# Kernel tuning notes

Measured on AMD Instinct MI355X. Metric: run time of the kernel, lower is better.

Reference implementation:

```python
import jax, jax.numpy as jnp
import numpy as np
import math

B, I, H = 8192, 1024, 1024


def setup_inputs() -> dict:
    key = jax.random.key(0)
    ks = jax.random.split(key, 16)
    stdv = 1.0 / math.sqrt(H)
    u = lambda k, shape: jax.random.uniform(k, shape, jnp.float32, -stdv, stdv)
    inp = {
        'xt': jax.random.normal(ks[0], (B, I), jnp.float32),
        'cx': jax.random.normal(ks[1], (B, H), jnp.float32),
        'hx': jax.random.normal(ks[2], (B, H), jnp.float32),
        'w_fg': u(ks[3], (H, I)), 'w_ig': u(ks[4], (H, I)),
        'w_og': u(ks[5], (H, I)), 'w_ci': u(ks[6], (H, I)),
        'r_fg': u(ks[7], (H, H)), 'r_ig': u(ks[8], (H, H)),
        'r_og': u(ks[9], (H, H)), 'r_ci': u(ks[10], (H, H)),
        'b_fg': u(ks[11], (H,)), 'b_ig': u(ks[12], (H,)),
        'b_og': u(ks[13], (H,)), 'b_ci': u(ks[14], (H,)),
    }
    return inp


def reference(xt, cx, hx, w_fg, w_ig, w_og, w_ci, r_fg, r_ig, r_og, r_ci,
              b_fg, b_ig, b_og, b_ci):
    # Fuse the four input matmuls and four recurrent matmuls into two GEMMs.
    W = jnp.concatenate([w_fg, w_ig, w_og, w_ci], axis=0)  # [4H, I]
    R = jnp.concatenate([r_fg, r_ig, r_og, r_ci], axis=0)  # [4H, H]
    b = jnp.concatenate([b_fg, b_ig, b_og, b_ci], axis=0)  # [4H]
    gates = xt @ W.T + hx @ R.T + b                         # [B, 4H]
    f, i, o, g = jnp.split(gates, 4, axis=-1)
    ft = jax.nn.sigmoid(f)
    it = jax.nn.sigmoid(i)
    ot = jax.nn.sigmoid(o)
    ct = ft * cx + it * jnp.tanh(g)
    ht = ot * jnp.tanh(ct)
    return (ht, ct)
```

## Files before the change

### kernel.cpp

```cpp
#include <hip/hip_runtime.h>

#define B_DIM 8192
#define H_DIM 1024
#define K_DIM 2048
#define N_DIM 4096
#define BH (B_DIM * H_DIM)
#define NT 32
#define TSZ (256 * 64)
#define HALFT (128 * 64)

using frag_ab = __attribute__((ext_vector_type(8))) short;
using frag_cd = __attribute__((ext_vector_type(4))) float;

__device__ __forceinline__ unsigned short f2bf(float f) {
  union { float f; unsigned u; } x; x.f = f;
  return (unsigned short)((x.u + 0x7fffu + ((x.u >> 16) & 1u)) >> 16);
}

__global__ __launch_bounds__(256) void convert_A_kernel(
    const float* __restrict__ xt, const float* __restrict__ hx,
    unsigned short* __restrict__ Ab) {
  int tid = blockIdx.x * 256 + threadIdx.x;
  int flat = tid * 4;
  int m = flat >> 11;
  int k = flat & 2047;
  const float* src = (k < 1024) ? (xt + m * 1024 + k)
                                : (hx + m * 1024 + (k - 1024));
  float4 v = *reinterpret_cast<const float4*>(src);
  ushort4 o;
  o.x = f2bf(v.x); o.y = f2bf(v.y); o.z = f2bf(v.z); o.w = f2bf(v.w);
  *reinterpret_cast<ushort4*>(Ab + flat) = o;
}

__global__ __launch_bounds__(256) void convert_B_kernel(
    const float* __restrict__ w0, const float* __restrict__ w1,
    const float* __restrict__ w2, const float* __restrict__ w3,
    const float* __restrict__ r0, const float* __restrict__ r1,
    const float* __restrict__ r2, const float* __restrict__ r3,
    unsigned short* __restrict__ Bb) {
  int tid = blockIdx.x * 256 + threadIdx.x;
  int flat = tid * 4;
  int n = flat >> 11;
  int k = flat & 2047;
  int tile = n >> 8, c = n & 255;
  int gate = (c >> 4) & 3;
  int h = tile * 64 + ((c >> 6) << 4) + (c & 15);
  const float* wb = (gate == 0) ? w0 : (gate == 1) ? w1 : (gate == 2) ? w2 : w3;
  const float* rb = (gate == 0) ? r0 : (gate == 1) ? r1 : (gate == 2) ? r2 : r3;
  const float* src = (k < 1024) ? (wb + h * 1024 + k)
                                : (rb + h * 1024 + (k - 1024));
  float4 v = *reinterpret_cast<const float4*>(src);
  ushort4 o;
  o.x = f2bf(v.x); o.y = f2bf(v.y); o.z = f2bf(v.z); o.w = f2bf(v.w);
  *reinterpret_cast<ushort4*>(Bb + flat) = o;
}

__device__ __forceinline__ void gload_lds16(const void* g, void* l) {
  __builtin_amdgcn_global_load_lds(
      (const __attribute__((address_space(1))) unsigned int*)g,
      (__attribute__((address_space(3))) unsigned int*)l, 16, 0, 0);
}

__device__ __forceinline__ frag_ab ldsr(const unsigned short* buf, int byteoff) {
  return *reinterpret_cast<const frag_ab*>(
      reinterpret_cast<const char*>(buf) + byteoff);
}

__device__ __forceinline__ float fast_sigmoid(float x) {
  return 1.f / (1.f + __expf(-x));
}
__device__ __forceinline__ float fast_tanh(float x) {
  return 1.f - 2.f / (__expf(2.f * x) + 1.f);
}

#define CBAR asm volatile("" ::: "memory")
#define SBAR do { CBAR; __builtin_amdgcn_s_barrier(); CBAR; } while (0)
#define SCHED0 __builtin_amdgcn_sched_barrier(0)

#define TILE_BODY(Ac, Bc, Anx, Bnx, tt, S1, S2, S3, S4, VM2, VM0)             \
  {                                                                            \
       \
    _Pragma("unroll") for (int m = 0; m < 4; ++m)                              \
        Af0[m] = ldsr(Ac, (arow + m * 16) * 128 + c0);                         \
    _Pragma("unroll") for (int n = 0; n < 4; ++n)                              \
        Bf0[n] = ldsr(Bc, (brow + n * 16) * 128 + c0);                         \
    if (S1) stage(Bg + 128 * K_DIM + (size_t)((tt) + 1) * 64, (Bnx) + HALFT);  \
    __builtin_amdgcn_s_setprio(1);                                             \
    _Pragma("unroll") for (int m = 0; m < 4; ++m)                              \
        _Pragma("unroll") for (int n = 0; n < 4; ++n)                          \
            acc[m][n] = __builtin_amdgcn_mfma_f32_16x16x32_bf16(               \
                Af0[m], Bf0[n], acc[m][n], 0, 0, 0);                           \
    __builtin_amdgcn_s_setprio(0);                                             \
    SCHED0;                                                                    \
    SBAR;                                                                      \
       \
    _Pragma("unroll") for (int m = 0; m < 4; ++m)                              \
        Af1[m] = ldsr(Ac, (arow + m * 16) * 128 + c1);                         \
    _Pragma("unroll") for (int n = 0; n < 4; ++n)                              \
        Bf1[n] = ldsr(Bc, (brow + n * 16) * 128 + c1);                         \
    if (S2) stage(Ag + (size_t)((tt) + 1) * 64, (Anx));                        \
    __builtin_amdgcn_s_setprio(1);                                             \
    _Pragma("unroll") for (int m = 0; m < 4; ++m)                              \
        _Pragma("unroll") for (int n = 0; n < 4; ++n)                          \
            acc[m][n] = __builtin_amdgcn_mfma_f32_16x16x32_bf16(               \
                Af1[m], Bf1[n], acc[m][n], 0, 0, 0);                           \
    __builtin_amdgcn_s_setprio(0);                                             \
    SCHED0;                                                                    \
    SBAR;                                                                      \
          \
    _Pragma("unroll") for (int m = 0; m < 4; ++m)                              \
        Af0[m] = ldsr(Ac, (arow + 64 + m * 16) * 128 + c0);                    \
    if (S3) stage(Ag + (size_t)((tt) + 1) * 64 + 128 * K_DIM, (Anx) + HALFT);  \
    __builtin_amdgcn_s_setprio(1);                                             \
    _Pragma("unroll") for (int m = 0; m < 4; ++m)                              \
        _Pragma("unroll") for (int n = 0; n < 4; ++n)                          \
            acc[4 + m][n] = __builtin_amdgcn_mfma_f32_16x16x32_bf16(           \
                Af0[m], Bf0[n], acc[4 + m][n], 0, 0, 0);                       \
    __builtin_amdgcn_s_setprio(0);                                             \
    SCHED0;                                                                    \
    SBAR;                                                                      \
     \
    _Pragma("unroll") for (int m = 0; m < 4; ++m)                              \
        Af1[m] = ldsr(Ac, (arow + 64 + m * 16) * 128 + c1);                    \
    if (S4) stage(Bg + (size_t)((tt) + 2) * 64, (Bc));                         \
    __builtin_amdgcn_s_setprio(1);                                             \
    _Pragma("unroll") for (int m = 0; m < 4; ++m)                              \
        _Pragma("unroll") for (int n = 0; n < 4; ++n)                          \
            acc[4 + m][n] = __builtin_amdgcn_mfma_f32_16x16x32_bf16(           \
                Af1[m], Bf1[n], acc[4 + m][n], 0, 0, 0);                       \
    __builtin_amdgcn_s_setprio(0);                                             \
    if (VM2) asm volatile("s_waitcnt vmcnt(2)" ::: "memory");                  \
    if (VM0) asm volatile("s_waitcnt vmcnt(0)" ::: "memory");                  \
    SCHED0;                                                                    \
    SBAR;                                                                      \
  }

__global__ __launch_bounds__(512, 2) void lstm_gemm_kernel(
    const unsigned short* __restrict__ Ab,
    const unsigned short* __restrict__ Bb,
    const float* __restrict__ cx,
    const float* __restrict__ b_f, const float* __restrict__ b_i,
    const float* __restrict__ b_o, const float* __restrict__ b_g,
    float* __restrict__ out) {
  extern __shared__ unsigned short smem[];
  unsigned short* const As0 = smem;
  unsigned short* const As1 = smem + TSZ;
  unsigned short* const Bs0 = smem + 2 * TSZ;
  unsigned short* const Bs1 = smem + 3 * TSZ;

  const int bid = blockIdx.x;
  const int swz = (bid & 7) * 64 + (bid >> 3);
  const int bm = swz >> 4;
  const int bn = swz & 15;

  const int tid = threadIdx.x;
  const int lane = tid & 63;
  const int wid = tid >> 6;
  const int wr = wid >> 2, wc = wid & 3;
  const int ln = lane & 15, kh = lane >> 4;

  const unsigned short* Ag = Ab + (size_t)(bm * 256) * K_DIM;
  const unsigned short* Bg = Bb + (size_t)(bn * 256) * K_DIM;

  const size_t gs0 = (size_t)(wid * 16 + (lane >> 3)) * K_DIM +
                     (((lane & 7) ^ (lane >> 3)) << 3);
  const size_t gs1 = gs0 + (size_t)8 * K_DIM;
  const int ld0 = wid * 2048 + lane * 16;
  const int ld1 = ld0 + 1024;
  auto stage = [&](const unsigned short* g, unsigned short* l) {
    gload_lds16(g + gs0, reinterpret_cast<char*>(l) + ld0);
    gload_lds16(g + gs1, reinterpret_cast<char*>(l) + ld1);
  };

  const int inv = (ln & 7) << 4;
  const int c0 = (kh * 16) ^ inv;
  const int c1 = (64 + kh * 16) ^ inv;
  const int arow = wr * 128 + ln;
  const int brow = wc * 64 + ln;

  frag_cd acc[8][4] = {};
  frag_ab Af0[4], Af1[4], Bf0[4], Bf1[4];

  stage(Ag, As0);
  stage(Ag + 128 * K_DIM, As0 + HALFT);
  stage(Bg, Bs0);
  stage(Bg + 128 * K_DIM, Bs0 + HALFT);
  stage(Bg + 64, Bs1);
  asm volatile("s_waitcnt vmcnt(2)" ::: "memory");
  SBAR;

  for (int u = 0; u < 15; ++u) {
    const int e = 2 * u;
    TILE_BODY(As0, Bs0, As1, Bs1, e, 1, 1, 1, 1, 1, 0);
    TILE_BODY(As1, Bs1, As0, Bs0, e + 1, 1, 1, 1, 1, 1, 0);
  }
  TILE_BODY(As0, Bs0, As1, Bs1, 30, 1, 1, 1, 0, 0, 1);
  TILE_BODY(As1, Bs1, As0, Bs0, 31, 0, 0, 0, 0, 0, 0);

  const int hcol = bn * 64 + wc * 16 + ln;
  const float bfv = b_f[hcol], biv = b_i[hcol], bov = b_o[hcol], bgv = b_g[hcol];
  const int row_base = bm * 256 + wr * 128 + kh * 4;
#pragma unroll
  for (int mi = 0; mi < 8; ++mi) {
#pragma unroll
    for (int j = 0; j < 4; ++j) {
      const int row = row_base + mi * 16 + j;
      float fp = acc[mi][0][j] + bfv;
      float ip = acc[mi][1][j] + biv;
      float op = acc[mi][2][j] + bov;
      float gp = acc[mi][3][j] + bgv;
      float ft = fast_sigmoid(fp);
      float it = fast_sigmoid(ip);
      float ot = fast_sigmoid(op);
      float gt = fast_tanh(gp);
      float cold = cx[(size_t)row * H_DIM + hcol];
      float ct = ft * cold + it * gt;
      float ht = ot * fast_tanh(ct);
      out[(size_t)row * H_DIM + hcol] = ht;
      out[BH + (size_t)row * H_DIM + hcol] = ct;
    }
  }
}

extern "C" void kernel_launch(void* const* d_in, const int* in_sizes, int n_in,
                              void* d_out, int out_size, void* d_ws, size_t ws_size,
                              hipStream_t stream) {
  const float* xt   = (const float*)d_in[0];
  const float* cxp  = (const float*)d_in[1];
  const float* hx   = (const float*)d_in[2];
  const float* w_fg = (const float*)d_in[3];
  const float* w_ig = (const float*)d_in[4];
  const float* w_og = (const float*)d_in[5];
  const float* w_ci = (const float*)d_in[6];
  const float* r_fg = (const float*)d_in[7];
  const float* r_ig = (const float*)d_in[8];
  const float* r_og = (const float*)d_in[9];
  const float* r_ci = (const float*)d_in[10];
  const float* b_fg = (const float*)d_in[11];
  const float* b_ig = (const float*)d_in[12];
  const float* b_og = (const float*)d_in[13];
  const float* b_ci = (const float*)d_in[14];

  unsigned short* Abf = (unsigned short*)d_ws;
  unsigned short* Bbf = Abf + (size_t)B_DIM * K_DIM;
  float* out = (float*)d_out;

  convert_A_kernel<<<dim3(B_DIM * K_DIM / 4 / 256), dim3(256), 0, stream>>>(
      xt, hx, Abf);
  convert_B_kernel<<<dim3(N_DIM * K_DIM / 4 / 256), dim3(256), 0, stream>>>(
      w_fg, w_ig, w_og, w_ci, r_fg, r_ig, r_og, r_ci, Bbf);
  lstm_gemm_kernel<<<dim3((B_DIM / 256) * (N_DIM / 256)), dim3(512),
                     131072, stream>>>(
      Abf, Bbf, cxp, b_fg, b_ig, b_og, b_ci, out);
}
```

Before: 157.5 us.

## Load A fragments directly from global in MFMA-ready layout, stage only B in LDS

The A-conversion kernel now writes bf16 activations in a fragment-tiled layout, so each wave loads its MFMA A operands straight from global memory into registers. Only B goes through LDS, which halves shared memory (64KB instead of 128KB) and cuts per-tile barriers from four to one. The cost is that A is read from global by each of the four column waves with no LDS sharing, relying on L2/L1 hits. The global-load latency also lands directly in the MFMA loop, with the vmcnt waits tuned to match.

```diff
diff --git a/kernel.cpp b/kernel.cpp
--- a/kernel.cpp
+++ b/kernel.cpp
@@ -6,11 +6,12 @@
 #define N_DIM 4096
 #define BH (B_DIM * H_DIM)
 #define NT 32
-#define TSZ (256 * 64)
-#define HALFT (128 * 64)
+#define BTSZ (256 * 64)
+#define HALFB (128 * 64)
 
 using frag_ab = __attribute__((ext_vector_type(8))) short;
 using frag_cd = __attribute__((ext_vector_type(4))) float;
+using short8 = __attribute__((ext_vector_type(8))) short;
 
 __device__ __forceinline__ unsigned short f2bf(float f) {
   union { float f; unsigned u; } x; x.f = f;
@@ -19,17 +20,21 @@
 
 __global__ __launch_bounds__(256) void convert_A_kernel(
     const float* __restrict__ xt, const float* __restrict__ hx,
-    unsigned short* __restrict__ Ab) {
-  int tid = blockIdx.x * 256 + threadIdx.x;
-  int flat = tid * 4;
-  int m = flat >> 11;
-  int k = flat & 2047;
-  const float* src = (k < 1024) ? (xt + m * 1024 + k)
-                                : (hx + m * 1024 + (k - 1024));
-  float4 v = *reinterpret_cast<const float4*>(src);
-  ushort4 o;
-  o.x = f2bf(v.x); o.y = f2bf(v.y); o.z = f2bf(v.z); o.w = f2bf(v.w);
-  *reinterpret_cast<ushort4*>(Ab + flat) = o;
+    unsigned short* __restrict__ At) {
+  int g = blockIdx.x * 256 + threadIdx.x;
+  int mt = g >> 12;
+  int kt = (g >> 6) & 63;
+  int l = g & 63;
+  int row = mt * 16 + (l & 15);
+  int col = kt * 32 + (l >> 4) * 8;
+  const float* src = (col < 1024) ? (xt + (size_t)row * 1024 + col)
+                                  : (hx + (size_t)row * 1024 + (col - 1024));
+  float4 v0 = *reinterpret_cast<const float4*>(src);
+  float4 v1 = *reinterpret_cast<const float4*>(src + 4);
+  short8 o;
+  o[0] = f2bf(v0.x); o[1] = f2bf(v0.y); o[2] = f2bf(v0.z); o[3] = f2bf(v0.w);
+  o[4] = f2bf(v1.x); o[5] = f2bf(v1.y); o[6] = f2bf(v1.z); o[7] = f2bf(v1.w);
+  *reinterpret_cast<short8*>(At + (size_t)g * 8) = o;
 }
 
 __global__ __launch_bounds__(256) void convert_B_kernel(
@@ -77,76 +82,73 @@
 #define SBAR do { CBAR; __builtin_amdgcn_s_barrier(); CBAR; } while (0)
 #define SCHED0 __builtin_amdgcn_sched_barrier(0)
 
-#define TILE_BODY(Ac, Bc, Anx, Bnx, tt, S1, S2, S3, S4, VM2, VM0)             \
+#define TILE_BODY(Bc, Bn, tt, S, P, VMQ)                                       \
   {                                                                            \
-       \
-    _Pragma("unroll") for (int m = 0; m < 4; ++m)                              \
-        Af0[m] = ldsr(Ac, (arow + m * 16) * 128 + c0);                         \
-    _Pragma("unroll") for (int n = 0; n < 4; ++n)                              \
-        Bf0[n] = ldsr(Bc, (brow + n * 16) * 128 + c0);                         \
-    if (S1) stage(Bg + 128 * K_DIM + (size_t)((tt) + 1) * 64, (Bnx) + HALFT);  \
+    if (S) {                                                                   \
+      stage(Bg + (size_t)((tt) + 1) * 64, (Bn));                               \
+      stage(Bg + (size_t)((tt) + 1) * 64 + 128 * K_DIM, (Bn) + HALFB);         \
+    }                                                                          \
+    SCHED0;                        \
+    _Pragma("unroll") for (int n = 0; n < 4; ++n) {                            \
+      Bf[n][0] = ldsr(Bc, (brow + n * 16) * 128 + c0);                         \
+      Bf[n][1] = ldsr(Bc, (brow + n * 16) * 128 + c1);                         \
+    }                                                                          \
+                 \
+    _Pragma("unroll") for (int m = 0; m < 4; ++m)                              \
+        Af1[m] = *reinterpret_cast<const frag_ab*>(                            \
+            awave + (size_t)m * 32768 + (2 * (tt) + 1) * 512);                 \
     __builtin_amdgcn_s_setprio(1);                                             \
     _Pragma("unroll") for (int m = 0; m < 4; ++m)                              \
         _Pragma("unroll") for (int n = 0; n < 4; ++n)                          \
             acc[m][n] = __builtin_amdgcn_mfma_f32_16x16x32_bf16(               \
-                Af0[m], Bf0[n], acc[m][n], 0, 0, 0);                           \
-    __builtin_amdgcn_s_setprio(0);                                             \
-    SCHED0;                                                                    \
-    SBAR;                                                                      \
-       \
-    _Pragma("unroll") for (int m = 0; m < 4; ++m)                              \
-        Af1[m] = ldsr(Ac, (arow + m * 16) * 128 + c1);                         \
-    _Pragma("unroll") for (int n = 0; n < 4; ++n)                              \
-        Bf1[n] = ldsr(Bc, (brow + n * 16) * 128 + c1);                         \
-    if (S2) stage(Ag + (size_t)((tt) + 1) * 64, (Anx));                        \
+                Af0[m], Bf[n][0], acc[m][n], 0, 0, 0);                         \
+    __builtin_amdgcn_s_setprio(0);                                             \
+                                 \
+    _Pragma("unroll") for (int m = 0; m < 4; ++m)                              \
+        Af0[m] = *reinterpret_cast<const frag_ab*>(                            \
+            awave + (size_t)(4 + m) * 32768 + (2 * (tt)) * 512);               \
     __builtin_amdgcn_s_setprio(1);                                             \
     _Pragma("unroll") for (int m = 0; m < 4; ++m)                              \
         _Pragma("unroll") for (int n = 0; n < 4; ++n)                          \
             acc[m][n] = __builtin_amdgcn_mfma_f32_16x16x32_bf16(               \
-                Af1[m], Bf1[n], acc[m][n], 0, 0, 0);                           \
-    __builtin_amdgcn_s_setprio(0);                                             \
-    SCHED0;                                                                    \
-    SBAR;                                                                      \
-          \
-    _Pragma("unroll") for (int m = 0; m < 4; ++m)                              \
-        Af0[m] = ldsr(Ac, (arow + 64 + m * 16) * 128 + c0);                    \
-    if (S3) stage(Ag + (size_t)((tt) + 1) * 64 + 128 * K_DIM, (Anx) + HALFT);  \
+                Af1[m], Bf[n][1], acc[m][n], 0, 0, 0);                         \
+    __builtin_amdgcn_s_setprio(0);                                             \
+                                 \
+    _Pragma("unroll") for (int m = 0; m < 4; ++m)                              \
+        Af1[m] = *reinterpret_cast<const frag_ab*>(                            \
+            awave + (size_t)(4 + m) * 32768 + (2 * (tt) + 1) * 512);           \
     __builtin_amdgcn_s_setprio(1);                                             \
     _Pragma("unroll") for (int m = 0; m < 4; ++m)                              \
         _Pragma("unroll") for (int n = 0; n < 4; ++n)                          \
             acc[4 + m][n] = __builtin_amdgcn_mfma_f32_16x16x32_bf16(           \
-                Af0[m], Bf0[n], acc[4 + m][n], 0, 0, 0);                       \
-    __builtin_amdgcn_s_setprio(0);                                             \
-    SCHED0;                                                                    \
-    SBAR;                                                                      \
-     \
-    _Pragma("unroll") for (int m = 0; m < 4; ++m)                              \
-        Af1[m] = ldsr(Ac, (arow + 64 + m * 16) * 128 + c1);                    \
-    if (S4) stage(Bg + (size_t)((tt) + 2) * 64, (Bc));                         \
+                Af0[m], Bf[n][0], acc[4 + m][n], 0, 0, 0);                     \
+    __builtin_amdgcn_s_setprio(0);                                             \
+                     \
+    if (P) _Pragma("unroll") for (int m = 0; m < 4; ++m)                       \
+        Af0[m] = *reinterpret_cast<const frag_ab*>(                            \
+            awave + (size_t)m * 32768 + (2 * (tt) + 2) * 512);                 \
     __builtin_amdgcn_s_setprio(1);                                             \
     _Pragma("unroll") for (int m = 0; m < 4; ++m)                              \
         _Pragma("unroll") for (int n = 0; n < 4; ++n)                          \
             acc[4 + m][n] = __builtin_amdgcn_mfma_f32_16x16x32_bf16(           \
-                Af1[m], Bf1[n], acc[4 + m][n], 0, 0, 0);                       \
-    __builtin_amdgcn_s_setprio(0);                                             \
-    if (VM2) asm volatile("s_waitcnt vmcnt(2)" ::: "memory");                  \
-    if (VM0) asm volatile("s_waitcnt vmcnt(0)" ::: "memory");                  \
-    SCHED0;                                                                    \
-    SBAR;                                                                      \
+                Af1[m], Bf[n][1], acc[4 + m][n], 0, 0, 0);                     \
+    __builtin_amdgcn_s_setprio(0);                                             \
+    if (VMQ) {                                                                 \
+      asm volatile("s_waitcnt vmcnt(16)" ::: "memory");    \
+      SBAR;                                                                    \
+    }                                                                          \
   }
 
 __global__ __launch_bounds__(512, 2) void lstm_gemm_kernel(
-    const unsigned short* __restrict__ Ab,
+    const unsigned short* __restrict__ At,
     const unsigned short* __restrict__ Bb,
     const float* __restrict__ cx,
     const float* __restrict__ b_f, const float* __restrict__ b_i,
     const float* __restrict__ b_o, const float* __restrict__ b_g,
     float* __restrict__ out) {
   extern __shared__ unsigned short smem[];
-  unsigned short* const As0 = smem;
-  unsigned short* const As1 = smem + TSZ;
-  unsigned short* const Bs0 = smem + 2 * TSZ;
-  unsigned short* const Bs1 = smem + 3 * TSZ;
+  unsigned short* const Bs0 = smem;
+  unsigned short* const Bs1 = smem + BTSZ;
 
   const int bid = blockIdx.x;
   const int swz = (bid & 7) * 64 + (bid >> 3);
@@ -159,7 +161,8 @@
   const int wr = wid >> 2, wc = wid & 3;
   const int ln = lane & 15, kh = lane >> 4;
 
-  const unsigned short* Ag = Ab + (size_t)(bm * 256) * K_DIM;
+  const unsigned short* awave =
+      At + ((size_t)(bm * 16 + wr * 8) * 64) * 512 + lane * 8;
   const unsigned short* Bg = Bb + (size_t)(bn * 256) * K_DIM;
 
   const size_t gs0 = (size_t)(wid * 16 + (lane >> 3)) * K_DIM +
@@ -175,27 +178,26 @@
   const int inv = (ln & 7) << 4;
   const int c0 = (kh * 16) ^ inv;
   const int c1 = (64 + kh * 16) ^ inv;
-  const int arow = wr * 128 + ln;
   const int brow = wc * 64 + ln;
 
   frag_cd acc[8][4] = {};
-  frag_ab Af0[4], Af1[4], Bf0[4], Bf1[4];
-
-  stage(Ag, As0);
-  stage(Ag + 128 * K_DIM, As0 + HALFT);
+  frag_ab Af0[4], Af1[4], Bf[4][2];
+
   stage(Bg, Bs0);
-  stage(Bg + 128 * K_DIM, Bs0 + HALFT);
-  stage(Bg + 64, Bs1);
-  asm volatile("s_waitcnt vmcnt(2)" ::: "memory");
+  stage(Bg + 128 * K_DIM, Bs0 + HALFB);
+#pragma unroll
+  for (int m = 0; m < 4; ++m)
+    Af0[m] = *reinterpret_cast<const frag_ab*>(awave + (size_t)m * 32768);
+  asm volatile("s_waitcnt vmcnt(4)" ::: "memory");
   SBAR;
 
   for (int u = 0; u < 15; ++u) {
     const int e = 2 * u;
-    TILE_BODY(As0, Bs0, As1, Bs1, e, 1, 1, 1, 1, 1, 0);
-    TILE_BODY(As1, Bs1, As0, Bs0, e + 1, 1, 1, 1, 1, 1, 0);
+    TILE_BODY(Bs0, Bs1, e, 1, 1, 1);
+    TILE_BODY(Bs1, Bs0, e + 1, 1, 1, 1);
   }
-  TILE_BODY(As0, Bs0, As1, Bs1, 30, 1, 1, 1, 0, 0, 1);
-  TILE_BODY(As1, Bs1, As0, Bs0, 31, 0, 0, 0, 0, 0, 0);
+  TILE_BODY(Bs0, Bs1, 30, 1, 1, 1);
+  TILE_BODY(Bs1, Bs0, 31, 0, 0, 0);
 
   const int hcol = bn * 64 + wc * 16 + ln;
   const float bfv = b_f[hcol], biv = b_i[hcol], bov = b_o[hcol], bgv = b_g[hcol];
@@ -241,15 +243,15 @@
   const float* b_og = (const float*)d_in[13];
   const float* b_ci = (const float*)d_in[14];
 
-  unsigned short* Abf = (unsigned short*)d_ws;
-  unsigned short* Bbf = Abf + (size_t)B_DIM * K_DIM;
+  unsigned short* Atf = (unsigned short*)d_ws;
+  unsigned short* Bbf = Atf + (size_t)B_DIM * K_DIM;
   float* out = (float*)d_out;
 
-  convert_A_kernel<<<dim3(B_DIM * K_DIM / 4 / 256), dim3(256), 0, stream>>>(
-      xt, hx, Abf);
+  convert_A_kernel<<<dim3(B_DIM * K_DIM / 8 / 256), dim3(256), 0, stream>>>(
+      xt, hx, Atf);
   convert_B_kernel<<<dim3(N_DIM * K_DIM / 4 / 256), dim3(256), 0, stream>>>(
       w_fg, w_ig, w_og, w_ci, r_fg, r_ig, r_og, r_ci, Bbf);
   lstm_gemm_kernel<<<dim3((B_DIM / 256) * (N_DIM / 256)), dim3(512),
-                     131072, stream>>>(
-      Abf, Bbf, cxp, b_fg, b_ig, b_og, b_ci, out);
-}
+                     65536, stream>>>(
+      Atf, Bbf, cxp, b_fg, b_ig, b_og, b_ci, out);
+}
```

Result: slower. 171.1 us (+8.7%).

## Move barriers before MFMA phases and use toggled LDS read pointers

Applied to the files above, without the earlier changes.

Each barrier in the tile body now sits right after the LDS fragment reads and the global-to-LDS stage issue, before the MFMA block, rather than after it. The sched_barrier fences are removed, so the compiler is free to interleave instructions. LDS read addresses become precomputed pointers flipped between double buffers with an XOR of 0x8000, and global source pointers advance incrementally. The aim is to cut address arithmetic and let barrier waits overlap with MFMA issue, at the risk of changing the ordering that protected buffers being overwritten while still in use.

```diff
diff --git a/kernel.cpp b/kernel.cpp
--- a/kernel.cpp
+++ b/kernel.cpp
@@ -61,11 +61,6 @@
       (__attribute__((address_space(3))) unsigned int*)l, 16, 0, 0);
 }
 
-__device__ __forceinline__ frag_ab ldsr(const unsigned short* buf, int byteoff) {
-  return *reinterpret_cast<const frag_ab*>(
-      reinterpret_cast<const char*>(buf) + byteoff);
-}
-
 __device__ __forceinline__ float fast_sigmoid(float x) {
   return 1.f / (1.f + __expf(-x));
 }
@@ -75,54 +70,52 @@
 
 #define CBAR asm volatile("" ::: "memory")
 #define SBAR do { CBAR; __builtin_amdgcn_s_barrier(); CBAR; } while (0)
-#define SCHED0 __builtin_amdgcn_sched_barrier(0)
-
-#define TILE_BODY(Ac, Bc, Anx, Bnx, tt, S1, S2, S3, S4, VM2, VM0)             \
+#define TOGG(p) (p) = (const char*)((size_t)(p) ^ 0x8000)
+
+#define TILE_BODY(Anx, Bnx, Bcur, S1, S2, S3, S4, VM2, VM0)                    \
   {                                                                            \
-       \
-    _Pragma("unroll") for (int m = 0; m < 4; ++m)                              \
-        Af0[m] = ldsr(Ac, (arow + m * 16) * 128 + c0);                         \
+                 \
+    _Pragma("unroll") for (int m = 0; m < 4; ++m)                              \
+        Af0[m] = *reinterpret_cast<const frag_ab*>(rdA0 + m * 2048);           \
     _Pragma("unroll") for (int n = 0; n < 4; ++n)                              \
-        Bf0[n] = ldsr(Bc, (brow + n * 16) * 128 + c0);                         \
-    if (S1) stage(Bg + 128 * K_DIM + (size_t)((tt) + 1) * 64, (Bnx) + HALFT);  \
+        Bf0[n] = *reinterpret_cast<const frag_ab*>(rdB0 + n * 2048);           \
+    if (S1) { stage(gB1, (Bnx) + HALFT); gB1 += 64; }                          \
+    SBAR;                                                                      \
     __builtin_amdgcn_s_setprio(1);                                             \
     _Pragma("unroll") for (int m = 0; m < 4; ++m)                              \
         _Pragma("unroll") for (int n = 0; n < 4; ++n)                          \
             acc[m][n] = __builtin_amdgcn_mfma_f32_16x16x32_bf16(               \
                 Af0[m], Bf0[n], acc[m][n], 0, 0, 0);                           \
     __builtin_amdgcn_s_setprio(0);                                             \
-    SCHED0;                                                                    \
-    SBAR;                                                                      \
-       \
-    _Pragma("unroll") for (int m = 0; m < 4; ++m)                              \
-        Af1[m] = ldsr(Ac, (arow + m * 16) * 128 + c1);                         \
+                                  \
+    _Pragma("unroll") for (int m = 0; m < 4; ++m)                              \
+        Af1[m] = *reinterpret_cast<const frag_ab*>(rdA1 + m * 2048);           \
     _Pragma("unroll") for (int n = 0; n < 4; ++n)                              \
-        Bf1[n] = ldsr(Bc, (brow + n * 16) * 128 + c1);                         \
-    if (S2) stage(Ag + (size_t)((tt) + 1) * 64, (Anx));                        \
+        Bf1[n] = *reinterpret_cast<const frag_ab*>(rdB1 + n * 2048);           \
+    if (S2) { stage(gA0, (Anx)); gA0 += 64; }                                  \
+    SBAR;                                                                      \
     __builtin_amdgcn_s_setprio(1);                                             \
     _Pragma("unroll") for (int m = 0; m < 4; ++m)                              \
         _Pragma("unroll") for (int n = 0; n < 4; ++n)                          \
             acc[m][n] = __builtin_amdgcn_mfma_f32_16x16x32_bf16(               \
                 Af1[m], Bf1[n], acc[m][n], 0, 0, 0);                           \
     __builtin_amdgcn_s_setprio(0);                                             \
-    SCHED0;                                                                    \
-    SBAR;                                                                      \
-          \
-    _Pragma("unroll") for (int m = 0; m < 4; ++m)                              \
-        Af0[m] = ldsr(Ac, (arow + 64 + m * 16) * 128 + c0);                    \
-    if (S3) stage(Ag + (size_t)((tt) + 1) * 64 + 128 * K_DIM, (Anx) + HALFT);  \
+                \
+    _Pragma("unroll") for (int m = 0; m < 4; ++m)                              \
+        Af0[m] = *reinterpret_cast<const frag_ab*>(rdA0 + 8192 + m * 2048);    \
+    if (S3) { stage(gA1, (Anx) + HALFT); gA1 += 64; }                          \
+    SBAR;                                                                      \
     __builtin_amdgcn_s_setprio(1);                                             \
     _Pragma("unroll") for (int m = 0; m < 4; ++m)                              \
         _Pragma("unroll") for (int n = 0; n < 4; ++n)                          \
             acc[4 + m][n] = __builtin_amdgcn_mfma_f32_16x16x32_bf16(           \
                 Af0[m], Bf0[n], acc[4 + m][n], 0, 0, 0);                       \
     __builtin_amdgcn_s_setprio(0);                                             \
-    SCHED0;                                                                    \
-    SBAR;                                                                      \
-     \
-    _Pragma("unroll") for (int m = 0; m < 4; ++m)                              \
-        Af1[m] = ldsr(Ac, (arow + 64 + m * 16) * 128 + c1);                    \
-    if (S4) stage(Bg + (size_t)((tt) + 2) * 64, (Bc));                         \
+        \
+    _Pragma("unroll") for (int m = 0; m < 4; ++m)                              \
+        Af1[m] = *reinterpret_cast<const frag_ab*>(rdA1 + 8192 + m * 2048);    \
+    if (S4) { stage(gB0, (Bcur)); gB0 += 64; }                                 \
+    SBAR;                                                                      \
     __builtin_amdgcn_s_setprio(1);                                             \
     _Pragma("unroll") for (int m = 0; m < 4; ++m)                              \
         _Pragma("unroll") for (int n = 0; n < 4; ++n)                          \
@@ -131,8 +124,7 @@
     __builtin_amdgcn_s_setprio(0);                                             \
     if (VM2) asm volatile("s_waitcnt vmcnt(2)" ::: "memory");                  \
     if (VM0) asm volatile("s_waitcnt vmcnt(0)" ::: "memory");                  \
-    SCHED0;                                                                    \
-    SBAR;                                                                      \
+    TOGG(rdA0); TOGG(rdA1); TOGG(rdB0); TOGG(rdB1);                            \
   }
 
 __global__ __launch_bounds__(512, 2) void lstm_gemm_kernel(
@@ -178,6 +170,16 @@
   const int arow = wr * 128 + ln;
   const int brow = wc * 64 + ln;
 
+  const char* rdA0 = reinterpret_cast<const char*>(As0) + arow * 128 + c0;
+  const char* rdA1 = reinterpret_cast<const char*>(As0) + arow * 128 + c1;
+  const char* rdB0 = reinterpret_cast<const char*>(Bs0) + brow * 128 + c0;
+  const char* rdB1 = reinterpret_cast<const char*>(Bs0) + brow * 128 + c1;
+
+  const unsigned short* gA0 = Ag + 64;
+  const unsigned short* gA1 = Ag + 64 + 128 * K_DIM;
+  const unsigned short* gB1 = Bg + 64 + 128 * K_DIM;
+  const unsigned short* gB0 = Bg + 128;
+
   frag_cd acc[8][4] = {};
   frag_ab Af0[4], Af1[4], Bf0[4], Bf1[4];
 
@@ -190,12 +192,11 @@
   SBAR;
 
   for (int u = 0; u < 15; ++u) {
-    const int e = 2 * u;
-    TILE_BODY(As0, Bs0, As1, Bs1, e, 1, 1, 1, 1, 1, 0);
-    TILE_BODY(As1, Bs1, As0, Bs0, e + 1, 1, 1, 1, 1, 1, 0);
+    TILE_BODY(As1, Bs1, Bs0, 1, 1, 1, 1, 1, 0);
+    TILE_BODY(As0, Bs0, Bs1, 1, 1, 1, 1, 1, 0);
   }
-  TILE_BODY(As0, Bs0, As1, Bs1, 30, 1, 1, 1, 0, 0, 1);
-  TILE_BODY(As1, Bs1, As0, Bs0, 31, 0, 0, 0, 0, 0, 0);
+  TILE_BODY(As1, Bs1, Bs0, 1, 1, 1, 0, 0, 1);
+  TILE_BODY(As0, Bs0, Bs1, 0, 0, 0, 0, 0, 0);
 
   const int hcol = bn * 64 + wc * 16 + ln;
   const float bfv = b_f[hcol], biv = b_i[hcol], bov = b_o[hcol], bgv = b_g[hcol];
```

New measurement: 178.3 us. 13.2% more time.
